# Optimization experiments

Measured on AMD Instinct MI355X. Metric: run time of the kernel, lower is better.

The kernel has to match this reference:

```python
import jax, jax.numpy as jnp
import numpy as np
from jax import lax

B, P, ENC, DEC, ATT, EMB, V, L = 64, 196, 2048, 512, 512, 512, 10000, 30


def setup_inputs() -> dict:
    key = jax.random.key(0)
    ks = jax.random.split(key, 24)
    s = 0.02
    encoder_out = jax.random.normal(ks[0], (B, P, ENC), dtype=jnp.float32)
    encoded_captions = jax.random.randint(ks[1], (B, L), 0, V, dtype=jnp.int64)
    caption_lengths = jax.random.randint(ks[2], (B, 1), 2, L + 1, dtype=jnp.int64)
    # ensure max decode length == L-1 (matches torch max(decode_lengths))
    caption_lengths = caption_lengths.at[0, 0].set(L)
    p = lambda k, sh: jax.random.normal(k, sh, dtype=jnp.float32) * s
    return {
        "encoder_out": encoder_out,
        "encoded_captions": encoded_captions,
        "caption_lengths": caption_lengths,
        "W_enc": p(ks[3], (ATT, ENC)), "b_enc": jnp.zeros((ATT,), jnp.float32),
        "W_dec": p(ks[4], (ATT, DEC)), "b_dec": jnp.zeros((ATT,), jnp.float32),
        "w_full": p(ks[5], (ATT,)), "b_full": jnp.zeros((), jnp.float32),
        "emb_table": jax.random.uniform(ks[6], (V, EMB), jnp.float32, -0.1, 0.1),
        "W_ih": p(ks[7], (4 * DEC, EMB + ENC)), "b_ih": jnp.zeros((4 * DEC,), jnp.float32),
        "W_hh": p(ks[8], (4 * DEC, DEC)), "b_hh": jnp.zeros((4 * DEC,), jnp.float32),
        "W_init_h": p(ks[9], (DEC, ENC)), "b_init_h": jnp.zeros((DEC,), jnp.float32),
        "W_init_c": p(ks[10], (DEC, ENC)), "b_init_c": jnp.zeros((DEC,), jnp.float32),
        "W_beta": p(ks[11], (ENC, DEC)), "b_beta": jnp.zeros((ENC,), jnp.float32),
        "W_fc": jax.random.uniform(ks[12], (V, DEC), jnp.float32, -0.1, 0.1),
        "b_fc": jnp.zeros((V,), jnp.float32),
    }


def reference(encoder_out, encoded_captions, caption_lengths,
              W_enc, b_enc, W_dec, b_dec, w_full, b_full, emb_table,
              W_ih, b_ih, W_hh, b_hh, W_init_h, b_init_h, W_init_c, b_init_c,
              W_beta, b_beta, W_fc, b_fc):
    lengths = caption_lengths[:, 0]
    sort_ind = jnp.argsort(-lengths)  # descending, stable
    enc = encoder_out[sort_ind]            # [B,P,ENC]
    caps = encoded_captions[sort_ind]      # [B,L]
    dec_lens = lengths[sort_ind] - 1       # [B]
    T = caps.shape[1] - 1

    embs = emb_table[caps]                 # [B,L,EMB]
    mean_enc = enc.mean(axis=1)
    h0 = mean_enc @ W_init_h.T + b_init_h
    c0 = mean_enc @ W_init_c.T + b_init_c
    # encoder attention projection is h-independent: compute once
    att1 = jnp.einsum('bpe,ae->bpa', enc, W_enc) + b_enc  # [B,P,ATT]

    def step(carry, xs):
        h, c = carry
        emb_t, mask_t = xs  # [B,EMB], [B] bool
        att2 = h @ W_dec.T + b_dec                              # [B,ATT]
        e = jax.nn.relu(att1 + att2[:, None, :]) @ w_full + b_full  # [B,P]
        alpha = jax.nn.softmax(e, axis=1)
        awe = jnp.einsum('bp,bpe->be', alpha, enc)              # [B,ENC]
        gate = jax.nn.sigmoid(h @ W_beta.T + b_beta)
        awe = gate * awe
        x = jnp.concatenate([emb_t, awe], axis=1)               # [B,EMB+ENC]
        gates = x @ W_ih.T + b_ih + h @ W_hh.T + b_hh           # [B,4D]
        i, f, g, o = jnp.split(gates, 4, axis=1)
        i, f, o = jax.nn.sigmoid(i), jax.nn.sigmoid(f), jax.nn.sigmoid(o)
        g = jnp.tanh(g)
        c_new = f * c + i * g
        h_new = o * jnp.tanh(c_new)
        preds = h_new @ W_fc.T + b_fc                           # [B,V]  (dropout: eval/identity)
        m = mask_t[:, None].astype(preds.dtype)
        return (h_new, c_new), (preds * m, alpha * m)

    mask = jnp.arange(T)[:, None] < dec_lens[None, :]           # [T,B]
    embs_t = jnp.swapaxes(embs[:, :T], 0, 1)                    # [T,B,EMB]
    _, (preds, alphas) = lax.scan(step, (h0, c0), (embs_t, mask))
    predictions = jnp.swapaxes(preds, 0, 1)                     # [B,T,V]
    alphas = jnp.swapaxes(alphas, 0, 1)                         # [B,T,P]
    return predictions, alphas, caps, dec_lens, sort_ind
```

## Files before the change

kernel.cpp:

```cpp
#include <hip/hip_runtime.h>
#include <hip/hip_bf16.h>
#include <math.h>
#include <float.h>

#define BDIM   64
#define PDIM   196
#define ENC    2048
#define DECD   512
#define ATTD   512
#define EMBD   512
#define VOC    10000
#define LCAP   30
#define TSTEPS 29

typedef __attribute__((ext_vector_type(8))) short s8v;
typedef __attribute__((ext_vector_type(4))) float f4v;

__device__ __forceinline__ float sigf(float x) { return 1.0f / (1.0f + expf(-x)); }
__device__ __forceinline__ float bf2f(ushort u) { return __uint_as_float(((uint)u) << 16); }

template <int MF, int NF, int NIT>
__device__ __forceinline__ void gemm_seg(const __hip_bfloat16* const* arow,
                                         const __hip_bfloat16* const* wrow,
                                         f4v acc[][NF]) {
    s8v aP[3][MF], bP[3][NF];
    auto LD = [&](int it, int slot) {
#pragma unroll
        for (int mi = 0; mi < MF; ++mi) aP[slot][mi] = *(const s8v*)(arow[mi] + it * 32);
#pragma unroll
        for (int ni = 0; ni < NF; ++ni) bP[slot][ni] = *(const s8v*)(wrow[ni] + it * 32);
    };
    LD(0, 0);
    if constexpr (NIT > 1) LD(1, 1);
#pragma unroll
    for (int it = 0; it < NIT; ++it) {
        if (it + 2 < NIT) LD(it + 2, (it + 2) % 3);
        const int s = it % 3;
#pragma unroll
        for (int mi = 0; mi < MF; ++mi)
#pragma unroll
            for (int ni = 0; ni < NF; ++ni)
                acc[mi][ni] = __builtin_amdgcn_mfma_f32_16x16x32_bf16(aP[s][mi], bP[s][ni], acc[mi][ni], 0, 0, 0);
    }
}


__device__ __forceinline__ void phase1(int bid, int tid,
    const __hip_bfloat16* hbuf, const __hip_bfloat16* Wb_bet,
    const __hip_bfloat16* Wb_dec, const __hip_bfloat16* Wb_hh, float* C_h) {
    const int l = tid & 63, c16 = l & 15, kg = l >> 4, w = tid >> 6;
    const int n0 = bid * 64;
    f4v acc[1][4];
#pragma unroll
    for (int ni = 0; ni < 4; ++ni) acc[0][ni] = (f4v)0.0f;
    const __hip_bfloat16* arow[1] = { hbuf + (size_t)(w * 16 + c16) * 512 + kg * 8 };
    const __hip_bfloat16* wrow[4];
#pragma unroll
    for (int ni = 0; ni < 4; ++ni) {
        int n = n0 + ni * 16 + c16;
        const __hip_bfloat16* wr;
        if (n < 2048)      wr = Wb_bet + (size_t)n * 512;
        else if (n < 2560) wr = Wb_dec + (size_t)(n - 2048) * 512;
        else               wr = Wb_hh + (size_t)(n - 2560) * 512;
        wrow[ni] = wr + kg * 8;
    }
    gemm_seg<1, 4, 16>(arow, wrow, acc);
#pragma unroll
    for (int ni = 0; ni < 4; ++ni)
#pragma unroll
        for (int i = 0; i < 4; ++i)
            C_h[(size_t)(w * 16 + kg * 4 + i) * 4608 + n0 + ni * 16 + c16] = acc[0][ni][i];
}

__device__ __forceinline__ void phase2(int bid, int tid, float* smem,
    const __hip_bfloat16* att1, const __hip_bfloat16* enc_s, const float* C_h,
    const float* w_full, const float* b_full, const float* b_dec,
    const float* b_beta, const int* dec_lens,
    __hip_bfloat16* awebuf, float* out_alphas, int t) {
    const int b = bid & 63, q = bid >> 6;
    const int l = tid & 63, w = tid >> 6;
    float* s_att2 = smem;
    float* s_wf   = smem + 512;
    float* s_e    = smem + 1024;
    float* red    = smem + 1280;
    float* s_part = smem + 1536;

    s_att2[tid]       = C_h[(size_t)b * 4608 + 2048 + tid]       + b_dec[tid];
    s_att2[tid + 256] = C_h[(size_t)b * 4608 + 2048 + 256 + tid] + b_dec[256 + tid];
    s_wf[tid]       = w_full[tid];
    s_wf[tid + 256] = w_full[tid + 256];
    __syncthreads();

    const float bf = b_full[0];
    const int a0 = l << 3;
    for (int p = w; p < PDIM; p += 4) {
        const ushort* row = (const ushort*)att1 + ((size_t)b * PDIM + p) * 512 + a0;
        s8v u = *(const s8v*)row;
        float s = 0.f;
#pragma unroll
        for (int i = 0; i < 8; ++i) {
            float x = bf2f((ushort)u[i]) + s_att2[a0 + i];
            s += fmaxf(x, 0.f) * s_wf[a0 + i];
        }
#pragma unroll
        for (int off = 32; off; off >>= 1) s += __shfl_xor(s, off);
        if (l == 0) s_e[p] = s + bf;
    }
    __syncthreads();

    float v = (tid < PDIM) ? s_e[tid] : -FLT_MAX;
    red[tid] = v;
    __syncthreads();
    for (int st = 128; st; st >>= 1) {
        if (tid < st) red[tid] = fmaxf(red[tid], red[tid + st]);
        __syncthreads();
    }
    float mx = red[0];
    __syncthreads();
    float ex = (tid < PDIM) ? expf(v - mx) : 0.f;
    red[tid] = ex;
    __syncthreads();
    for (int st = 128; st; st >>= 1) {
        if (tid < st) red[tid] += red[tid + st];
        __syncthreads();
    }
    float inv = 1.f / red[0];
    __syncthreads();
    if (tid < PDIM) {
        float al = ex * inv;
        s_e[tid] = al;
        if (q == 0)
            out_alphas[(size_t)b * (TSTEPS * PDIM) + (size_t)t * PDIM + tid] =
                (t < dec_lens[b]) ? al : 0.f;
    }
    __syncthreads();

    const int c0 = q * 512 + l * 8;
    const ushort* ep = (const ushort*)enc_s + (size_t)b * (PDIM * ENC) + c0;
    float a8[8];
#pragma unroll
    for (int i = 0; i < 8; ++i) a8[i] = 0.f;
    for (int p = w * 49; p < w * 49 + 49; ++p) {
        float al = s_e[p];
        s8v u = *(const s8v*)(ep + (size_t)p * ENC);
#pragma unroll
        for (int i = 0; i < 8; ++i) a8[i] += al * bf2f((ushort)u[i]);
    }
#pragma unroll
    for (int i = 0; i < 8; ++i) s_part[w * 512 + l * 8 + i] = a8[i];
    __syncthreads();
#pragma unroll
    for (int u2 = 0; u2 < 2; ++u2) {
        int cc = tid * 2 + u2;
        float s = s_part[cc] + s_part[512 + cc] + s_part[1024 + cc] + s_part[1536 + cc];
        int gcol = q * 512 + cc;
        float gate = sigf(C_h[(size_t)b * 4608 + gcol] + b_beta[gcol]);
        awebuf[(size_t)b * 2048 + gcol] = __float2bfloat16(s * gate);
    }
}

__device__ __forceinline__ void phase3(int bid, int tid, float* smem,
    const __hip_bfloat16* awebuf, const __hip_bfloat16* embs_all,
    const __hip_bfloat16* Wb_ih, const float* C_h,
    const float* b_ih, const float* b_hh,
    float* cbuf, __hip_bfloat16* hbuf, __hip_bfloat16* hstore, int t) {
    const int l = tid & 63, c16 = l & 15, kg = l >> 4, w = tid >> 6;
    const int j0 = bid * 16;
    f4v acc[4][1];
#pragma unroll
    for (int mi = 0; mi < 4; ++mi) acc[mi][0] = (f4v)0.0f;
    const __hip_bfloat16* arow[4];
    const __hip_bfloat16* wrow[1];
    const __hip_bfloat16* wbase = Wb_ih + (size_t)(512 * w + j0 + c16) * 2560;
#pragma unroll
    for (int mi = 0; mi < 4; ++mi)
        arow[mi] = embs_all + ((size_t)t * 64 + mi * 16 + c16) * 512 + kg * 8;
    wrow[0] = wbase + kg * 8;
    gemm_seg<4, 1, 16>(arow, wrow, acc);
#pragma unroll
    for (int mi = 0; mi < 4; ++mi)
        arow[mi] = awebuf + (size_t)(mi * 16 + c16) * 2048 + kg * 8;
    wrow[0] = wbase + 512 + kg * 8;
    gemm_seg<4, 1, 64>(arow, wrow, acc);
#pragma unroll
    for (int mi = 0; mi < 4; ++mi)
#pragma unroll
        for (int i = 0; i < 4; ++i)
            smem[w * 1024 + (mi * 16 + kg * 4 + i) * 16 + c16] = acc[mi][0][i];
    __syncthreads();
#pragma unroll
    for (int u2 = 0; u2 < 4; ++u2) {
        int pid = u2 * 256 + tid;
        int b = pid >> 4, jj = pid & 15;
        float vg[4];
#pragma unroll
        for (int g = 0; g < 4; ++g) {
            int col = 512 * g + j0 + jj;
            vg[g] = smem[g * 1024 + b * 16 + jj]
                  + C_h[(size_t)b * 4608 + 2560 + col]
                  + b_ih[col] + b_hh[col];
        }
        float i_ = sigf(vg[0]), f_ = sigf(vg[1]), gg = tanhf(vg[2]), o_ = sigf(vg[3]);
        int cidx = b * 512 + j0 + jj;
        float cn = f_ * cbuf[cidx] + i_ * gg;
        cbuf[cidx] = cn;
        __hip_bfloat16 hb = __float2bfloat16(o_ * tanhf(cn));
        hbuf[cidx] = hb;
        hstore[(size_t)t * (64 * 512) + cidx] = hb;
    }
}

__global__ __launch_bounds__(256) void p1_kernel(
    const __hip_bfloat16* hbuf, const __hip_bfloat16* Wb_bet,
    const __hip_bfloat16* Wb_dec, const __hip_bfloat16* Wb_hh, float* C_h) {
    phase1(blockIdx.x, threadIdx.x, hbuf, Wb_bet, Wb_dec, Wb_hh, C_h);
}
__global__ __launch_bounds__(256) void p2_kernel(
    const __hip_bfloat16* att1, const __hip_bfloat16* enc_s, const float* C_h,
    const float* w_full, const float* b_full, const float* b_dec,
    const float* b_beta, const int* dec_lens,
    __hip_bfloat16* awebuf, float* out_alphas, int t) {
    __shared__ float smem[4096];
    phase2(blockIdx.x, threadIdx.x, smem, att1, enc_s, C_h, w_full, b_full,
           b_dec, b_beta, dec_lens, awebuf, out_alphas, t);
}
__global__ __launch_bounds__(256) void p3_kernel(
    const __hip_bfloat16* awebuf, const __hip_bfloat16* embs_all,
    const __hip_bfloat16* Wb_ih, const float* C_h,
    const float* b_ih, const float* b_hh,
    float* cbuf, __hip_bfloat16* hbuf, __hip_bfloat16* hstore, int t) {
    __shared__ float smem[4096];
    phase3(blockIdx.x, threadIdx.x, smem, awebuf, embs_all, Wb_ih, C_h,
           b_ih, b_hh, cbuf, hbuf, hstore, t);
}

__global__ void sort_kernel(const int* __restrict__ cap_len,
                            const int* __restrict__ caps,
                            int* __restrict__ sort_ind,
                            int* __restrict__ dec_lens,
                            int* __restrict__ caps_s,
                            float* __restrict__ out_caps,
                            float* __restrict__ out_dlen,
                            float* __restrict__ out_sind) {
    int i = threadIdx.x;
    __shared__ int len[BDIM];
    len[i] = cap_len[i];
    __syncthreads();
    int li = len[i];
    int r = 0;
    for (int j = 0; j < BDIM; ++j) {
        int lj = len[j];
        if (lj > li || (lj == li && j < i)) ++r;
    }
    sort_ind[r] = i;
    dec_lens[r] = li - 1;
    out_sind[r] = (float)i;
    out_dlen[r] = (float)(li - 1);
    for (int tt = 0; tt < LCAP; ++tt) {
        int v = caps[i * LCAP + tt];
        caps_s[r * LCAP + tt] = v;
        out_caps[r * LCAP + tt] = (float)v;
    }
}

__global__ __launch_bounds__(256) void conv_enc_kernel(const float* __restrict__ enc,
                                                       const int* __restrict__ sort_ind,
                                                       __hip_bfloat16* __restrict__ enc_s,
                                                       float* __restrict__ mean_enc) {
    int b = blockIdx.y, tid = threadIdx.x;
    int e = (blockIdx.x << 8) + tid;
    const float* ep = enc + (size_t)sort_ind[b] * (PDIM * ENC) + e;
    __hip_bfloat16* op = enc_s + (size_t)b * (PDIM * ENC) + e;
    float s = 0.f;
    for (int p = 0; p < PDIM; ++p) {
        float v = ep[(size_t)p * ENC];
        s += v;
        op[(size_t)p * ENC] = __float2bfloat16(v);
    }
    mean_enc[(size_t)b * ENC + e] = s * (1.0f / (float)PDIM);
}

__global__ __launch_bounds__(256) void f2b_kernel(const float* __restrict__ src,
                                                  __hip_bfloat16* __restrict__ dst, int n) {
    int i = blockIdx.x * 256 + threadIdx.x;
    if (i < n) dst[i] = __float2bfloat16(src[i]);
}

__global__ __launch_bounds__(256) void h0b_kernel(const float* __restrict__ h0f,
                                                  __hip_bfloat16* __restrict__ hbuf) {
    int idx = blockIdx.x * 256 + threadIdx.x;
    hbuf[idx] = __float2bfloat16(h0f[idx]);
}

__global__ __launch_bounds__(256) void embgather_kernel(
    const float* __restrict__ emb_table, const int* __restrict__ caps_s,
    __hip_bfloat16* __restrict__ embs_all) {
    int b = blockIdx.x, t = blockIdx.y;
    int cap = caps_s[b * LCAP + t];
    int j = threadIdx.x << 1;
    float2 e = *(const float2*)(emb_table + (size_t)cap * EMBD + j);
    __hip_bfloat16 eb[2];
    eb[0] = __float2bfloat16(e.x); eb[1] = __float2bfloat16(e.y);
    *(uint*)(embs_all + ((size_t)t * 64 + b) * 512 + j) = *(uint*)eb;
}

__global__ __launch_bounds__(256) void gemm32_k(
    const float* __restrict__ A, int lda,
    const float* __restrict__ W0, const float* __restrict__ bias0,
    float* __restrict__ C, int ldc, int K) {
    __shared__ float As[16][64];
    __shared__ float Ws[16][64];
    const int tid = threadIdx.x;
    const int tx = tid & 15, ty = tid >> 4;
    const int bn0 = blockIdx.x * 64;
    const int lr = tid >> 2;
    const int lk = (tid & 3) << 2;
    const float* Arow = A + (size_t)lr * lda;
    const int wn = bn0 + lr;
    float acc[4][4];
#pragma unroll
    for (int i = 0; i < 4; ++i)
#pragma unroll
        for (int j = 0; j < 4; ++j) acc[i][j] = 0.f;
    for (int k0 = 0; k0 < K; k0 += 16) {
        float4 av = *(const float4*)(Arow + k0 + lk);
        float4 wv = *(const float4*)(W0 + (size_t)wn * K + k0 + lk);
        __syncthreads();
        As[lk + 0][lr] = av.x; As[lk + 1][lr] = av.y;
        As[lk + 2][lr] = av.z; As[lk + 3][lr] = av.w;
        Ws[lk + 0][lr] = wv.x; Ws[lk + 1][lr] = wv.y;
        Ws[lk + 2][lr] = wv.z; Ws[lk + 3][lr] = wv.w;
        __syncthreads();
#pragma unroll
        for (int kk = 0; kk < 16; ++kk) {
            const float4 a = *(const float4*)&As[kk][ty << 2];
            const float4 w = *(const float4*)&Ws[kk][tx << 2];
            acc[0][0] += a.x * w.x; acc[0][1] += a.x * w.y; acc[0][2] += a.x * w.z; acc[0][3] += a.x * w.w;
            acc[1][0] += a.y * w.x; acc[1][1] += a.y * w.y; acc[1][2] += a.y * w.z; acc[1][3] += a.y * w.w;
            acc[2][0] += a.z * w.x; acc[2][1] += a.z * w.y; acc[2][2] += a.z * w.z; acc[2][3] += a.z * w.w;
            acc[3][0] += a.w * w.x; acc[3][1] += a.w * w.y; acc[3][2] += a.w * w.z; acc[3][3] += a.w * w.w;
        }
    }
#pragma unroll
    for (int i = 0; i < 4; ++i) {
        int row = (ty << 2) + i;
#pragma unroll
        for (int j = 0; j < 4; ++j) {
            int col = bn0 + (tx << 2) + j;
            C[(size_t)row * ldc + col] = acc[i][j] + bias0[col];
        }
    }
}

__global__ __launch_bounds__(256) void att1_gemm(
    const __hip_bfloat16* __restrict__ A, const __hip_bfloat16* __restrict__ W,
    const float* __restrict__ bias, __hip_bfloat16* __restrict__ C) {
    const int tid = threadIdx.x;
    const int l = tid & 63, c16 = l & 15, kg = l >> 4, w = tid >> 6;
    const int m0 = blockIdx.x * 64 + w * 16, n0 = blockIdx.y * 64;
    f4v acc[1][4];
#pragma unroll
    for (int ni = 0; ni < 4; ++ni) acc[0][ni] = (f4v)0.0f;
    const __hip_bfloat16* arow[1] = { A + (size_t)(m0 + c16) * ENC + kg * 8 };
    const __hip_bfloat16* wrow[4];
#pragma unroll
    for (int ni = 0; ni < 4; ++ni)
        wrow[ni] = W + (size_t)(n0 + ni * 16 + c16) * ENC + kg * 8;
    gemm_seg<1, 4, 64>(arow, wrow, acc);
#pragma unroll
    for (int ni = 0; ni < 4; ++ni)
#pragma unroll
        for (int i = 0; i < 4; ++i) {
            int r = m0 + kg * 4 + i;
            int c = n0 + ni * 16 + c16;
            C[(size_t)r * 512 + c] = __float2bfloat16(acc[0][ni][i] + bias[c]);
        }
}

__global__ __launch_bounds__(64) void predsb_gemm(
    const __hip_bfloat16* __restrict__ Hs,
    const __hip_bfloat16* __restrict__ Wfc,
    const float* __restrict__ bias,
    const int* __restrict__ dec_lens,
    float* __restrict__ out) {
    const int l = threadIdx.x, c16 = l & 15, kg = l >> 4;
    const int n0 = blockIdx.x * 64, m0 = blockIdx.y * 32;
    f4v acc[2][4];
#pragma unroll
    for (int mi = 0; mi < 2; ++mi)
#pragma unroll
        for (int ni = 0; ni < 4; ++ni) acc[mi][ni] = (f4v)0.0f;
    const __hip_bfloat16* arow[2];
#pragma unroll
    for (int mi = 0; mi < 2; ++mi)
        arow[mi] = Hs + (size_t)(m0 + mi * 16 + c16) * 512 + kg * 8;
    const __hip_bfloat16* wrow[4];
#pragma unroll
    for (int ni = 0; ni < 4; ++ni) {
        int n = n0 + ni * 16 + c16;
        int nn = (n < VOC) ? n : (VOC - 1);
        wrow[ni] = Wfc + (size_t)nn * 512 + kg * 8;
    }
    gemm_seg<2, 4, 16>(arow, wrow, acc);
#pragma unroll
    for (int mi = 0; mi < 2; ++mi)
#pragma unroll
        for (int ni = 0; ni < 4; ++ni)
#pragma unroll
            for (int i = 0; i < 4; ++i) {
                int r = m0 + mi * 16 + kg * 4 + i;
                int c = n0 + ni * 16 + c16;
                if (c < VOC) {
                    int tt = r >> 6, b = r & 63;
                    float v = acc[mi][ni][i] + bias[c];
                    out[(size_t)b * (TSTEPS * VOC) + (size_t)tt * VOC + c] =
                        (tt < dec_lens[b]) ? v : 0.f;
                }
            }
}

extern "C" void kernel_launch(void* const* d_in, const int* in_sizes, int n_in,
                              void* d_out, int out_size, void* d_ws, size_t ws_size,
                              hipStream_t stream) {
    const float* enc      = (const float*)d_in[0];
    const int*   caps     = (const int*)d_in[1];
    const int*   clen     = (const int*)d_in[2];
    const float* W_enc    = (const float*)d_in[3];
    const float* b_enc    = (const float*)d_in[4];
    const float* W_dec    = (const float*)d_in[5];
    const float* b_dec    = (const float*)d_in[6];
    const float* w_full   = (const float*)d_in[7];
    const float* b_full   = (const float*)d_in[8];
    const float* emb_tab  = (const float*)d_in[9];
    const float* W_ih     = (const float*)d_in[10];
    const float* b_ih     = (const float*)d_in[11];
    const float* W_hh     = (const float*)d_in[12];
    const float* b_hh     = (const float*)d_in[13];
    const float* W_init_h = (const float*)d_in[14];
    const float* b_init_h = (const float*)d_in[15];
    const float* W_init_c = (const float*)d_in[16];
    const float* b_init_c = (const float*)d_in[17];
    const float* W_beta   = (const float*)d_in[18];
    const float* b_beta   = (const float*)d_in[19];
    const float* W_fc     = (const float*)d_in[20];
    const float* b_fc     = (const float*)d_in[21];

    float* out_pred = (float*)d_out;
    float* out_alph = out_pred + (size_t)BDIM * TSTEPS * VOC;
    float* out_caps = out_alph + (size_t)BDIM * TSTEPS * PDIM;
    float* out_dlen = out_caps + BDIM * LCAP;
    float* out_sind = out_dlen + BDIM;

    char* p = (char*)d_ws;
    auto carve = [&](size_t bytes) { char* r = p; p += (bytes + 255) & ~(size_t)255; return r; };
    int* sort_ind = (int*)carve(64 * 4);
    int* dec_lens = (int*)carve(64 * 4);
    int* caps_s   = (int*)carve(64 * LCAP * 4);
    float* cbuf   = (float*)carve((size_t)64 * 512 * 4);
    float* C_h    = (float*)carve((size_t)64 * 4608 * 4);
    float* mean_e = (float*)carve((size_t)64 * ENC * 4);
    float* h0f    = (float*)carve((size_t)64 * 512 * 4);
    __hip_bfloat16* hbuf   = (__hip_bfloat16*)carve((size_t)64 * 512 * 2);
    __hip_bfloat16* awebuf = (__hip_bfloat16*)carve((size_t)64 * 2048 * 2);
    __hip_bfloat16* hstore = (__hip_bfloat16*)carve((size_t)TSTEPS * 64 * 512 * 2);
    __hip_bfloat16* enc_s  = (__hip_bfloat16*)carve((size_t)64 * PDIM * ENC * 2);
    __hip_bfloat16* att1   = (__hip_bfloat16*)carve((size_t)64 * PDIM * 512 * 2);
    __hip_bfloat16* Wb_enc = (__hip_bfloat16*)carve((size_t)512 * 2048 * 2);
    __hip_bfloat16* Wb_bet = (__hip_bfloat16*)carve((size_t)2048 * 512 * 2);
    __hip_bfloat16* Wb_dec = (__hip_bfloat16*)carve((size_t)512 * 512 * 2);
    __hip_bfloat16* Wb_ih  = (__hip_bfloat16*)carve((size_t)2048 * 2560 * 2);
    __hip_bfloat16* Wb_hh  = (__hip_bfloat16*)carve((size_t)2048 * 512 * 2);
    __hip_bfloat16* Wb_fc  = (__hip_bfloat16*)carve((size_t)VOC * 512 * 2);
    __hip_bfloat16* embs_all = Wb_enc;

    sort_kernel<<<1, 64, 0, stream>>>(clen, caps, sort_ind, dec_lens, caps_s,
                                      out_caps, out_dlen, out_sind);
    conv_enc_kernel<<<dim3(8, 64), 256, 0, stream>>>(enc, sort_ind, enc_s, mean_e);
    f2b_kernel<<<(512 * 2048 + 255) / 256, 256, 0, stream>>>(W_enc, Wb_enc, 512 * 2048);
    f2b_kernel<<<(2048 * 512 + 255) / 256, 256, 0, stream>>>(W_beta, Wb_bet, 2048 * 512);
    f2b_kernel<<<(512 * 512 + 255) / 256, 256, 0, stream>>>(W_dec, Wb_dec, 512 * 512);
    f2b_kernel<<<(2048 * 2560 + 255) / 256, 256, 0, stream>>>(W_ih, Wb_ih, 2048 * 2560);
    f2b_kernel<<<(2048 * 512 + 255) / 256, 256, 0, stream>>>(W_hh, Wb_hh, 2048 * 512);
    f2b_kernel<<<(VOC * 512 + 255) / 256, 256, 0, stream>>>(W_fc, Wb_fc, VOC * 512);

    gemm32_k<<<dim3(8, 1), 256, 0, stream>>>(mean_e, ENC, W_init_h, b_init_h, h0f, 512, ENC);
    gemm32_k<<<dim3(8, 1), 256, 0, stream>>>(mean_e, ENC, W_init_c, b_init_c, cbuf, 512, ENC);
    h0b_kernel<<<128, 256, 0, stream>>>(h0f, hbuf);

    att1_gemm<<<dim3(196, 8), 256, 0, stream>>>(enc_s, Wb_enc, b_enc, att1);

    embgather_kernel<<<dim3(64, TSTEPS), 256, 0, stream>>>(emb_tab, caps_s, embs_all);

    for (int t = 0; t < TSTEPS; ++t) {
        p1_kernel<<<72, 256, 0, stream>>>(hbuf, Wb_bet, Wb_dec, Wb_hh, C_h);
        p2_kernel<<<256, 256, 0, stream>>>(att1, enc_s, C_h, w_full, b_full,
                                           b_dec, b_beta, dec_lens, awebuf,
                                           out_alph, t);
        p3_kernel<<<32, 256, 0, stream>>>(awebuf, embs_all, Wb_ih, C_h,
                                          b_ih, b_hh, cbuf, hbuf, hstore, t);
    }

    predsb_gemm<<<dim3(160, 58), 64, 0, stream>>>(hstore, Wb_fc, b_fc, dec_lens, out_pred);
}
```

Measured before the change: 3.639 ms.

## Batch loads in attention phase, split-K in LSTM gate phase, bigger att1 tiles

In the attention phase, each wave now issues eight row loads at once, for both the score pass and the weighted-sum pass, so more memory requests are in flight. The LSTM gate phase now runs 512 threads per block and splits the K dimension across two wave groups, summing the partial results in shared memory. This doubles parallelism on the 32-block latency-bound step. The att1 GEMM computes 128-row tiles per block with early exit for extra blocks, which raises reuse of the weight tiles. The risks are more register pressure from the eight-vector buffers and twice the shared memory in the gate phase.

After: 3.286 ms. -9.7%, faster.

```diff
diff --git a/kernel.cpp b/kernel.cpp
--- a/kernel.cpp
+++ b/kernel.cpp
@@ -93,18 +93,38 @@
 
     const float bf = b_full[0];
     const int a0 = l << 3;
-    for (int p = w; p < PDIM; p += 4) {
-        const ushort* row = (const ushort*)att1 + ((size_t)b * PDIM + p) * 512 + a0;
-        s8v u = *(const s8v*)row;
+    const int p0 = w * 49;
+    const ushort* abase = (const ushort*)att1 + ((size_t)b * PDIM) * 512 + a0;
+    {
+        s8v u[8];
+#pragma unroll 1
+        for (int pb = 0; pb < 48; pb += 8) {
+#pragma unroll
+            for (int i = 0; i < 8; ++i)
+                u[i] = *(const s8v*)(abase + (size_t)(p0 + pb + i) * 512);
+#pragma unroll
+            for (int i = 0; i < 8; ++i) {
+                float s = 0.f;
+#pragma unroll
+                for (int j = 0; j < 8; ++j) {
+                    float x = bf2f((ushort)u[i][j]) + s_att2[a0 + j];
+                    s += fmaxf(x, 0.f) * s_wf[a0 + j];
+                }
+#pragma unroll
+                for (int off = 32; off; off >>= 1) s += __shfl_xor(s, off);
+                if (l == 0) s_e[p0 + pb + i] = s + bf;
+            }
+        }
+        s8v ut = *(const s8v*)(abase + (size_t)(p0 + 48) * 512);
         float s = 0.f;
 #pragma unroll
-        for (int i = 0; i < 8; ++i) {
-            float x = bf2f((ushort)u[i]) + s_att2[a0 + i];
-            s += fmaxf(x, 0.f) * s_wf[a0 + i];
+        for (int j = 0; j < 8; ++j) {
+            float x = bf2f((ushort)ut[j]) + s_att2[a0 + j];
+            s += fmaxf(x, 0.f) * s_wf[a0 + j];
         }
 #pragma unroll
         for (int off = 32; off; off >>= 1) s += __shfl_xor(s, off);
-        if (l == 0) s_e[p] = s + bf;
+        if (l == 0) s_e[p0 + 48] = s + bf;
     }
     __syncthreads();
 
@@ -140,11 +160,24 @@
     float a8[8];
 #pragma unroll
     for (int i = 0; i < 8; ++i) a8[i] = 0.f;
-    for (int p = w * 49; p < w * 49 + 49; ++p) {
-        float al = s_e[p];
-        s8v u = *(const s8v*)(ep + (size_t)p * ENC);
-#pragma unroll
-        for (int i = 0; i < 8; ++i) a8[i] += al * bf2f((ushort)u[i]);
+    {
+        s8v u[8];
+#pragma unroll 1
+        for (int pb = 0; pb < 48; pb += 8) {
+#pragma unroll
+            for (int i = 0; i < 8; ++i)
+                u[i] = *(const s8v*)(ep + (size_t)(p0 + pb + i) * ENC);
+#pragma unroll
+            for (int i = 0; i < 8; ++i) {
+                float al = s_e[p0 + pb + i];
+#pragma unroll
+                for (int j = 0; j < 8; ++j) a8[j] += al * bf2f((ushort)u[i][j]);
+            }
+        }
+        s8v ut = *(const s8v*)(ep + (size_t)(p0 + 48) * ENC);
+        float al = s_e[p0 + 48];
+#pragma unroll
+        for (int j = 0; j < 8; ++j) a8[j] += al * bf2f((ushort)ut[j]);
     }
 #pragma unroll
     for (int i = 0; i < 8; ++i) s_part[w * 512 + l * 8 + i] = a8[i];
@@ -165,23 +198,32 @@
     const float* b_ih, const float* b_hh,
     float* cbuf, __hip_bfloat16* hbuf, __hip_bfloat16* hstore, int t) {
     const int l = tid & 63, c16 = l & 15, kg = l >> 4, w = tid >> 6;
+    const int g = w & 3, kh = w >> 2;
     const int j0 = bid * 16;
     f4v acc[4][1];
 #pragma unroll
     for (int mi = 0; mi < 4; ++mi) acc[mi][0] = (f4v)0.0f;
     const __hip_bfloat16* arow[4];
     const __hip_bfloat16* wrow[1];
-    const __hip_bfloat16* wbase = Wb_ih + (size_t)(512 * w + j0 + c16) * 2560;
-#pragma unroll
-    for (int mi = 0; mi < 4; ++mi)
-        arow[mi] = embs_all + ((size_t)t * 64 + mi * 16 + c16) * 512 + kg * 8;
-    wrow[0] = wbase + kg * 8;
-    gemm_seg<4, 1, 16>(arow, wrow, acc);
-#pragma unroll
-    for (int mi = 0; mi < 4; ++mi)
-        arow[mi] = awebuf + (size_t)(mi * 16 + c16) * 2048 + kg * 8;
-    wrow[0] = wbase + 512 + kg * 8;
-    gemm_seg<4, 1, 64>(arow, wrow, acc);
+    const __hip_bfloat16* wbase = Wb_ih + (size_t)(512 * g + j0 + c16) * 2560;
+    if (kh == 0) {
+#pragma unroll
+        for (int mi = 0; mi < 4; ++mi)
+            arow[mi] = embs_all + ((size_t)t * 64 + mi * 16 + c16) * 512 + kg * 8;
+        wrow[0] = wbase + kg * 8;
+        gemm_seg<4, 1, 16>(arow, wrow, acc);
+#pragma unroll
+        for (int mi = 0; mi < 4; ++mi)
+            arow[mi] = awebuf + (size_t)(mi * 16 + c16) * 2048 + kg * 8;
+        wrow[0] = wbase + 512 + kg * 8;
+        gemm_seg<4, 1, 24>(arow, wrow, acc);
+    } else {
+#pragma unroll
+        for (int mi = 0; mi < 4; ++mi)
+            arow[mi] = awebuf + (size_t)(mi * 16 + c16) * 2048 + 768 + kg * 8;
+        wrow[0] = wbase + 1280 + kg * 8;
+        gemm_seg<4, 1, 40>(arow, wrow, acc);
+    }
 #pragma unroll
     for (int mi = 0; mi < 4; ++mi)
 #pragma unroll
@@ -189,20 +231,21 @@
             smem[w * 1024 + (mi * 16 + kg * 4 + i) * 16 + c16] = acc[mi][0][i];
     __syncthreads();
 #pragma unroll
-    for (int u2 = 0; u2 < 4; ++u2) {
-        int pid = u2 * 256 + tid;
+    for (int u2 = 0; u2 < 2; ++u2) {
+        int pid = u2 * 512 + tid;
         int b = pid >> 4, jj = pid & 15;
+        int idx = b * 16 + jj;
         float vg[4];
 #pragma unroll
-        for (int g = 0; g < 4; ++g) {
-            int col = 512 * g + j0 + jj;
-            vg[g] = smem[g * 1024 + b * 16 + jj]
-                  + C_h[(size_t)b * 4608 + 2560 + col]
-                  + b_ih[col] + b_hh[col];
+        for (int gg2 = 0; gg2 < 4; ++gg2) {
+            int col = 512 * gg2 + j0 + jj;
+            vg[gg2] = smem[gg2 * 1024 + idx] + smem[(4 + gg2) * 1024 + idx]
+                    + C_h[(size_t)b * 4608 + 2560 + col]
+                    + b_ih[col] + b_hh[col];
         }
-        float i_ = sigf(vg[0]), f_ = sigf(vg[1]), gg = tanhf(vg[2]), o_ = sigf(vg[3]);
+        float i_ = sigf(vg[0]), f_ = sigf(vg[1]), gt = tanhf(vg[2]), o_ = sigf(vg[3]);
         int cidx = b * 512 + j0 + jj;
-        float cn = f_ * cbuf[cidx] + i_ * gg;
+        float cn = f_ * cbuf[cidx] + i_ * gt;
         cbuf[cidx] = cn;
         __hip_bfloat16 hb = __float2bfloat16(o_ * tanhf(cn));
         hbuf[cidx] = hb;
@@ -224,12 +267,12 @@
     phase2(blockIdx.x, threadIdx.x, smem, att1, enc_s, C_h, w_full, b_full,
            b_dec, b_beta, dec_lens, awebuf, out_alphas, t);
 }
-__global__ __launch_bounds__(256) void p3_kernel(
+__global__ __launch_bounds__(512) void p3_kernel(
     const __hip_bfloat16* awebuf, const __hip_bfloat16* embs_all,
     const __hip_bfloat16* Wb_ih, const float* C_h,
     const float* b_ih, const float* b_hh,
     float* cbuf, __hip_bfloat16* hbuf, __hip_bfloat16* hstore, int t) {
-    __shared__ float smem[4096];
+    __shared__ float smem[8192];
     phase3(blockIdx.x, threadIdx.x, smem, awebuf, embs_all, Wb_ih, C_h,
            b_ih, b_hh, cbuf, hbuf, hstore, t);
 }
@@ -355,26 +398,35 @@
 __global__ __launch_bounds__(256) void att1_gemm(
     const __hip_bfloat16* __restrict__ A, const __hip_bfloat16* __restrict__ W,
     const float* __restrict__ bias, __hip_bfloat16* __restrict__ C) {
+    const int bx = blockIdx.x;
+    if (bx >= 98) return;
     const int tid = threadIdx.x;
     const int l = tid & 63, c16 = l & 15, kg = l >> 4, w = tid >> 6;
-    const int m0 = blockIdx.x * 64 + w * 16, n0 = blockIdx.y * 64;
-    f4v acc[1][4];
-#pragma unroll
-    for (int ni = 0; ni < 4; ++ni) acc[0][ni] = (f4v)0.0f;
-    const __hip_bfloat16* arow[1] = { A + (size_t)(m0 + c16) * ENC + kg * 8 };
+    const int m0 = bx * 128 + w * 32, n0 = blockIdx.y * 64;
+    f4v acc[2][4];
+#pragma unroll
+    for (int mi = 0; mi < 2; ++mi)
+#pragma unroll
+        for (int ni = 0; ni < 4; ++ni) acc[mi][ni] = (f4v)0.0f;
+    const __hip_bfloat16* arow[2];
+#pragma unroll
+    for (int mi = 0; mi < 2; ++mi)
+        arow[mi] = A + (size_t)(m0 + mi * 16 + c16) * ENC + kg * 8;
     const __hip_bfloat16* wrow[4];
 #pragma unroll
     for (int ni = 0; ni < 4; ++ni)
         wrow[ni] = W + (size_t)(n0 + ni * 16 + c16) * ENC + kg * 8;
-    gemm_seg<1, 4, 64>(arow, wrow, acc);
-#pragma unroll
-    for (int ni = 0; ni < 4; ++ni)
-#pragma unroll
-        for (int i = 0; i < 4; ++i) {
-            int r = m0 + kg * 4 + i;
-            int c = n0 + ni * 16 + c16;
-            C[(size_t)r * 512 + c] = __float2bfloat16(acc[0][ni][i] + bias[c]);
-        }
+    gemm_seg<2, 4, 64>(arow, wrow, acc);
+#pragma unroll
+    for (int mi = 0; mi < 2; ++mi)
+#pragma unroll
+        for (int ni = 0; ni < 4; ++ni)
+#pragma unroll
+            for (int i = 0; i < 4; ++i) {
+                int r = m0 + mi * 16 + kg * 4 + i;
+                int c = n0 + ni * 16 + c16;
+                C[(size_t)r * 512 + c] = __float2bfloat16(acc[mi][ni][i] + bias[c]);
+            }
 }
 
 __global__ __launch_bounds__(64) void predsb_gemm(
@@ -487,7 +539,7 @@
     gemm32_k<<<dim3(8, 1), 256, 0, stream>>>(mean_e, ENC, W_init_c, b_init_c, cbuf, 512, ENC);
     h0b_kernel<<<128, 256, 0, stream>>>(h0f, hbuf);
 
-    att1_gemm<<<dim3(196, 8), 256, 0, stream>>>(enc_s, Wb_enc, b_enc, att1);
+    att1_gemm<<<dim3(104, 8), 256, 0, stream>>>(enc_s, Wb_enc, b_enc, att1);
 
     embgather_kernel<<<dim3(64, TSTEPS), 256, 0, stream>>>(emb_tab, caps_s, embs_all);
 
@@ -496,7 +548,7 @@
         p2_kernel<<<256, 256, 0, stream>>>(att1, enc_s, C_h, w_full, b_full,
                                            b_dec, b_beta, dec_lens, awebuf,
                                            out_alph, t);
-        p3_kernel<<<32, 256, 0, stream>>>(awebuf, embs_all, Wb_ih, C_h,
+        p3_kernel<<<32, 512, 0, stream>>>(awebuf, embs_all, Wb_ih, C_h,
                                           b_ih, b_hh, cbuf, hbuf, hstore, t);
     }
 
```
